# Kernel optimization log

Hardware: AMD Instinct MI355X
Metric: run time of the kernel (lower is better)

The kernel has to match this reference:

```python
import jax, jax.numpy as jnp
import numpy as np

B, S, D = 4, 2048, 768
H, K = 12, 64

def setup_inputs() -> dict:
    key = jax.random.key(0)
    k1, k2, k3, k4 = jax.random.split(key, 4)
    x = jax.random.normal(k1, (B, S, D), dtype=jnp.float32)
    Wq = jax.random.normal(k2, (H, D, K), dtype=jnp.float32) * 0.02
    Wk = jax.random.normal(k3, (H, D, K), dtype=jnp.float32) * 0.02
    Wv = jax.random.normal(k4, (H, D, K), dtype=jnp.float32) * 0.02
    return {"x": x, "Wq": Wq, "Wk": Wk, "Wv": Wv}

def reference(x, Wq, Wk, Wv):
    # per-head projections (batched over heads): [B,H,S,K]
    q = jnp.einsum('bsd,hdk->bhsk', x, Wq)
    k = jnp.einsum('bsd,hdk->bhsk', x, Wk)
    v = jnp.einsum('bsd,hdk->bhsk', x, Wv)
    scale = 1.0 / jnp.sqrt(jnp.float32(q.shape[-1]))
    scores = jnp.einsum('bhsk,bhtk->bhst', q, k) * scale  # [B,H,S,S]
    causal = jnp.tril(jnp.ones((x.shape[1], x.shape[1]), dtype=bool))
    scores = jnp.where(causal, scores, jnp.float32(-jnp.inf))
    wei = jax.nn.softmax(scores, axis=-1)
    out = jnp.einsum('bhst,bhtk->bhsk', wei, v)  # [B,H,S,K]
    # concat heads on last dim, matching torch.cat([head(x)...], dim=-1)
    b, h, s, kk = out.shape
    return out.transpose(0, 2, 1, 3).reshape(b, s, h * kk)
```

## Files before the change

kernel.cpp:

```cpp
#include <hip/hip_runtime.h>
#include <math.h>

#define BB 4
#define SS 2048
#define DD 768
#define HH 12
#define KK 64

#define NPROJ 3
#define HK    (HH * KK)
#define NCOLS (NPROJ * HK)
#define MROWS (BB * SS)
#define PER   (BB * HH * SS * KK)

typedef __attribute__((ext_vector_type(8))) short bf16x8;
typedef __attribute__((ext_vector_type(4))) short bf16x4;
typedef __attribute__((ext_vector_type(4))) float f32x4;
typedef __attribute__((ext_vector_type(16))) float f32x16;

static __device__ __forceinline__ short f2bf(float f) {
  union { float f; unsigned u; } v;
  v.f = f;
  unsigned r = (v.u + 0x7fff + ((v.u >> 16) & 1)) >> 16;
  return (short)r;
}

static __device__ __forceinline__ unsigned cvtpk(float lo, float hi) {
  unsigned r;
  asm("v_cvt_pk_bf16_f32 %0, %1, %2" : "=v"(r) : "v"(lo), "v"(hi));
  return r;
}

static __device__ __forceinline__ float fexp2(float x) {
#if __has_builtin(__builtin_amdgcn_exp2f)
  return __builtin_amdgcn_exp2f(x);
#else
  return exp2f(x);
#endif
}

__global__ __launch_bounds__(256) void conv_x(const float* __restrict__ x,
                                              short* __restrict__ xbf) {
  int i = (blockIdx.x * 256 + threadIdx.x) * 4;
  float4 v = *(const float4*)(x + i);
  bf16x4 o = {f2bf(v.x), f2bf(v.y), f2bf(v.z), f2bf(v.w)};
  *(bf16x4*)(xbf + i) = o;
}

__global__ __launch_bounds__(256) void conv_w(const float* __restrict__ Wq,
                                              const float* __restrict__ Wk,
                                              const float* __restrict__ Wv,
                                              short* __restrict__ wbf) {
  int o = blockIdx.x * 256 + threadIdx.x;
  int n = o / DD, d = o % DD;
  int proj = n / HK;
  int hk = n % HK;
  int h = hk >> 6, k = hk & 63;
  const float* W = proj == 0 ? Wq : (proj == 1 ? Wk : Wv);
  float v = W[(size_t)h * DD * KK + (size_t)d * KK + k];
  if (proj == 0) v *= 0.125f * 1.44269504088896340736f;
  wbf[o] = f2bf(v);
}

__global__ __launch_bounds__(256) void qkv_gemm(const short* __restrict__ xbf,
                                                const short* __restrict__ wbf,
                                                short* __restrict__ qkv) {
  __shared__ short smem[128 * 128];
  short* As = smem;
  short* Bs = smem + 128 * 64;
  int bm = blockIdx.x & 63, bn = blockIdx.x >> 6;
  int m0 = bm * 128, n0 = bn * 128;
  int tid = threadIdx.x, lane = tid & 63, wid = tid >> 6;
  int li = lane & 15, lg = lane >> 4;
  int wm = wid >> 1, wn = wid & 1;

  f32x4 acc[4][4];
  #pragma unroll
  for (int mi = 0; mi < 4; ++mi)
    #pragma unroll
    for (int ni = 0; ni < 4; ++ni)
      acc[mi][ni] = (f32x4){0.f, 0.f, 0.f, 0.f};

  int rowoff = lane >> 3;
  int kpsw = ((lane & 7) ^ rowoff) * 8;

  for (int kt = 0; kt < DD / 64; ++kt) {
    #pragma unroll
    for (int j = 0; j < 4; ++j) {
      int eb = wid * 2048 + j * 512;
      int row = (eb >> 6) + rowoff;
      __builtin_amdgcn_global_load_lds(
          (const __attribute__((address_space(1))) void*)(
              xbf + (size_t)(m0 + row) * DD + kt * 64 + kpsw),
          (__attribute__((address_space(3))) void*)(As + eb), 16, 0, 0);
      __builtin_amdgcn_global_load_lds(
          (const __attribute__((address_space(1))) void*)(
              wbf + (size_t)(n0 + row) * DD + kt * 64 + kpsw),
          (__attribute__((address_space(3))) void*)(Bs + eb), 16, 0, 0);
    }
    __syncthreads();

    #pragma unroll
    for (int kk = 0; kk < 2; ++kk) {
      bf16x8 af[4], bfr[4];
      #pragma unroll
      for (int mi = 0; mi < 4; ++mi)
        af[mi] = *(const bf16x8*)(As + (wm * 64 + mi * 16 + li) * 64 +
                                  (((kk * 4 + lg) ^ (li & 7)) << 3));
      #pragma unroll
      for (int ni = 0; ni < 4; ++ni)
        bfr[ni] = *(const bf16x8*)(Bs + (wn * 64 + ni * 16 + li) * 64 +
                                   (((kk * 4 + lg) ^ (li & 7)) << 3));
      #pragma unroll
      for (int mi = 0; mi < 4; ++mi)
        #pragma unroll
        for (int ni = 0; ni < 4; ++ni)
          acc[mi][ni] = __builtin_amdgcn_mfma_f32_16x16x32_bf16(
              af[mi], bfr[ni], acc[mi][ni], 0, 0, 0);
    }
    __syncthreads();
  }

  int proj = n0 / HK;
  int hk0 = n0 % HK;
  int h0 = hk0 >> 6;

  if (proj == 2) {
    #pragma unroll
    for (int ni = 0; ni < 4; ++ni) {
      int ncol = n0 + wn * 64 + ni * 16 + li;
      int hk = ncol % HK;
      int h = hk >> 6, k = hk & 63;
      #pragma unroll
      for (int mi = 0; mi < 4; ++mi) {
        int mrow0 = m0 + wm * 64 + mi * 16 + lg * 4;
        int b = mrow0 >> 11, s = mrow0 & 2047;
        bf16x4 o = {f2bf(acc[mi][ni][0]), f2bf(acc[mi][ni][1]),
                    f2bf(acc[mi][ni][2]), f2bf(acc[mi][ni][3])};
        *(bf16x4*)(qkv + 2 * (size_t)PER +
                   ((size_t)(b * HH + h) * KK + k) * SS + s) = o;
      }
    }
  } else {
    short* Cs = smem;
    #pragma unroll
    for (int ni = 0; ni < 4; ++ni) {
      int nl = wn * 64 + ni * 16 + li;
      int slot = nl >> 3, nlo = nl & 7;
      #pragma unroll
      for (int mi = 0; mi < 4; ++mi) {
        int ml0 = wm * 64 + mi * 16 + lg * 4;
        #pragma unroll
        for (int r = 0; r < 4; ++r) {
          int ml = ml0 + r;
          Cs[ml * 128 + ((slot ^ (ml & 7)) << 3) + nlo] =
              f2bf(acc[mi][ni][r]);
        }
      }
    }
    __syncthreads();
    int sl = tid & 7;
    #pragma unroll
    for (int p = 0; p < 8; ++p) {
      int line = p * 32 + (tid >> 3);
      int hh = line >> 7, mrow = line & 127;
      bf16x8 v = *(const bf16x8*)&Cs[mrow * 128 +
                                     (((hh * 8 + sl) ^ (mrow & 7)) << 3)];
      int gm = m0 + mrow;
      int b = gm >> 11, s = gm & 2047;
      *(bf16x8*)(qkv + (size_t)proj * PER +
                 ((size_t)(b * HH + h0 + hh) * SS + s) * KK + sl * 8) = v;
    }
  }
}

static __device__ __forceinline__ void attn_step_lds(
    const short* Kt, const short* Vv, const bf16x8* qf, bool diag, int h2,
    int lq, int hi, float& lsum, f32x16& acc0, f32x16& acc1) {
  int x7 = lq & 7;
  bf16x8 kf[4];
  {
    int kbase = (h2 * 32 + lq) * 64;
    #pragma unroll
    for (int c = 0; c < 4; ++c)
      kf[c] = *(const bf16x8*)&Kt[kbase + (((2 * c + hi) ^ x7)) * 8];
  }
  bf16x8 vf[2][2];
  #pragma unroll
  for (int m2 = 0; m2 < 2; ++m2) {
    int vbase = (32 * m2 + lq) * 64;
    #pragma unroll
    for (int c = 0; c < 2; ++c)
      vf[m2][c] =
          *(const bf16x8*)&Vv[vbase + (((h2 * 4 + 2 * c + hi) ^ x7)) * 8];
  }

  f32x16 sc;
  #pragma unroll
  for (int r = 0; r < 16; ++r) sc[r] = 0.f;
  #pragma unroll
  for (int c = 0; c < 4; ++c)
    sc = __builtin_amdgcn_mfma_f32_32x32x16_bf16(kf[c], qf[c], sc, 0, 0, 0);

  if (diag) {
    #pragma unroll
    for (int r = 0; r < 16; ++r) {
      int crow = (r & 3) + 8 * (r >> 2) + 4 * hi;
      if (crow > lq) sc[r] = -INFINITY;
    }
  }

  float p[16];
  #pragma unroll
  for (int r = 0; r < 16; ++r) p[r] = fexp2(sc[r]);

  float s8[8];
  #pragma unroll
  for (int r = 0; r < 8; ++r) s8[r] = p[2 * r] + p[2 * r + 1];
  lsum += ((s8[0] + s8[1]) + (s8[2] + s8[3])) +
          ((s8[4] + s8[5]) + (s8[6] + s8[7]));

  bf16x8 pf[2];
  #pragma unroll
  for (int c = 0; c < 2; ++c) {
    unsigned a0u = cvtpk(p[8 * c + 0], p[8 * c + 1]);
    unsigned b0u = cvtpk(p[8 * c + 4], p[8 * c + 5]);
    unsigned a1u = cvtpk(p[8 * c + 2], p[8 * c + 3]);
    unsigned b1u = cvtpk(p[8 * c + 6], p[8 * c + 7]);
    asm volatile("v_permlane32_swap_b32 %0, %1" : "+v"(a0u), "+v"(b0u));
    asm volatile("v_permlane32_swap_b32 %0, %1" : "+v"(a1u), "+v"(b1u));
    union { unsigned u[4]; bf16x8 v; } pu;
    pu.u[0] = a0u; pu.u[1] = a1u; pu.u[2] = b0u; pu.u[3] = b1u;
    pf[c] = pu.v;
  }

  acc0 = __builtin_amdgcn_mfma_f32_32x32x16_bf16(vf[0][0], pf[0], acc0, 0, 0, 0);
  acc0 = __builtin_amdgcn_mfma_f32_32x32x16_bf16(vf[0][1], pf[1], acc0, 0, 0, 0);
  acc1 = __builtin_amdgcn_mfma_f32_32x32x16_bf16(vf[1][0], pf[0], acc1, 0, 0, 0);
  acc1 = __builtin_amdgcn_mfma_f32_32x32x16_bf16(vf[1][1], pf[1], acc1, 0, 0, 0);
}

__global__ __launch_bounds__(256) void attn_kernel(
    const short* __restrict__ qkv, float* __restrict__ out) {
  __shared__ short tile[2][8192];

  int tid = threadIdx.x;
  int wid = tid >> 6, lane = tid & 63;
  int bid = blockIdx.x;
  int qb = 15 - bid / 48;
  int bh = bid % 48;
  int b = bh / HH, h = bh % HH;
  int Q0 = qb * 128;
  int s0w = Q0 + 32 * wid;
  int lq = lane & 31, hi = lane >> 5;

  const short* Qb = qkv + (size_t)bh * SS * KK;
  const short* Kb = qkv + (size_t)PER + (size_t)bh * SS * KK;
  const short* Vt = qkv + 2 * (size_t)PER + (size_t)bh * KK * SS;

  bf16x8 qf[4];
  #pragma unroll
  for (int c = 0; c < 4; ++c)
    qf[c] = *(const bf16x8*)(Qb + (size_t)(s0w + lq) * KK + c * 16 + hi * 8);

  f32x16 acc0, acc1;
  #pragma unroll
  for (int r = 0; r < 16; ++r) { acc0[r] = 0.f; acc1[r] = 0.f; }
  float lsum = 0.f;

  int srow = tid >> 3;
  int sl2 = (tid & 7) ^ (srow & 7);
  int ldsK = wid * 512;

  const int tmax = 2 * qb + 1;

  #define STAGE(bf_, t_)                                                       \
    {                                                                          \
      int kt0 = (t_) * 64;                                                     \
      _Pragma("unroll")                                                        \
      for (int i = 0; i < 2; ++i) {                                            \
        __builtin_amdgcn_global_load_lds(                                      \
            (const __attribute__((address_space(1))) void*)(                   \
                Kb + (size_t)(kt0 + i * 32 + srow) * KK + sl2 * 8),            \
            (__attribute__((address_space(3))) void*)(&tile[bf_][i * 2048 +    \
                                                                 ldsK]),       \
            16, 0, 0);                                                         \
        __builtin_amdgcn_global_load_lds(                                      \
            (const __attribute__((address_space(1))) void*)(                   \
                Vt + (size_t)(i * 32 + srow) * SS + kt0 + sl2 * 8),            \
            (__attribute__((address_space(3))) void*)(&tile[bf_][4096 +        \
                                                                 i * 2048 +    \
                                                                 ldsK]),       \
            16, 0, 0);                                                         \
      }                                                                        \
    }

  STAGE(0, 0);

  for (int t = 0; t <= tmax; ++t) {
    int cur = t & 1;
    if (t < tmax) {
      STAGE(cur ^ 1, t + 1);
      asm volatile("s_waitcnt vmcnt(4)" ::: "memory");
    } else {
      asm volatile("s_waitcnt vmcnt(0)" ::: "memory");
    }
    __builtin_amdgcn_s_barrier();

    const short* Kt = &tile[cur][0];
    const short* Vv = &tile[cur][4096];
    int kt0 = t * 64;
    #pragma unroll
    for (int h2 = 0; h2 < 2; ++h2) {
      int ks = kt0 + 32 * h2;
      if (ks <= s0w)
        attn_step_lds(Kt, Vv, qf, ks == s0w, h2, lq, hi, lsum, acc0, acc1);
    }
    __builtin_amdgcn_s_barrier();
  }
  #undef STAGE

  lsum += __shfl_xor(lsum, 32, 64);
  float inv = 1.0f / lsum;
  float* orow = out + ((size_t)(b * SS + s0w + lq)) * HK + h * KK;
  #pragma unroll
  for (int g = 0; g < 4; ++g) {
    int kd = 8 * g + 4 * hi;
    float4 w0 = {acc0[g * 4 + 0] * inv, acc0[g * 4 + 1] * inv,
                 acc0[g * 4 + 2] * inv, acc0[g * 4 + 3] * inv};
    float4 w1 = {acc1[g * 4 + 0] * inv, acc1[g * 4 + 1] * inv,
                 acc1[g * 4 + 2] * inv, acc1[g * 4 + 3] * inv};
    *(float4*)(orow + kd) = w0;
    *(float4*)(orow + 32 + kd) = w1;
  }
}

extern "C" void kernel_launch(void* const* d_in, const int* in_sizes, int n_in,
                              void* d_out, int out_size, void* d_ws,
                              size_t ws_size, hipStream_t stream) {
  const float* x  = (const float*)d_in[0];
  const float* Wq = (const float*)d_in[1];
  const float* Wk = (const float*)d_in[2];
  const float* Wv = (const float*)d_in[3];
  short* ws  = (short*)d_ws;
  short* qkv = ws;
  short* xbf = ws + (size_t)3 * PER;
  short* wbf = xbf + (size_t)MROWS * DD;
  float* o   = (float*)d_out;

  conv_x<<<(MROWS * DD) / 4 / 256, 256, 0, stream>>>(x, xbf);
  conv_w<<<(NCOLS * DD) / 256, 256, 0, stream>>>(Wq, Wk, Wv, wbf);
  qkv_gemm<<<(MROWS / 128) * (NCOLS / 128), 256, 0, stream>>>(xbf, wbf, qkv);
  attn_kernel<<<48 * 16, 256, 0, stream>>>(ws, o);
}
```

Baseline: 111.7 us.

## Double-buffer QKV GEMM LDS tiles and remap block order for L2 locality

The QKV projection GEMM now uses two LDS buffers, so the async global-to-LDS loads for the next K tile are issued before computing on the current one, with vmcnt waits and raw barriers instead of full syncthreads. Block indices are also remapped so that consecutive blocks interleave over tile groups, which is meant to spread work and improve cache reuse across CUs. The cost is doubled LDS (64KB), which may lower occupancy, and reliance on hand-placed waitcnt counts for correctness.

```diff
diff --git a/kernel.cpp b/kernel.cpp
--- a/kernel.cpp
+++ b/kernel.cpp
@@ -65,10 +65,10 @@
 __global__ __launch_bounds__(256) void qkv_gemm(const short* __restrict__ xbf,
                                                 const short* __restrict__ wbf,
                                                 short* __restrict__ qkv) {
-  __shared__ short smem[128 * 128];
-  short* As = smem;
-  short* Bs = smem + 128 * 64;
-  int bm = blockIdx.x & 63, bn = blockIdx.x >> 6;
+  __shared__ short smem[4 * 128 * 64];
+  int bid = blockIdx.x;
+  int tile = (bid & 7) * 144 + (bid >> 3);
+  int bm = tile & 63, bn = tile >> 6;
   int m0 = bm * 128, n0 = bn * 128;
   int tid = threadIdx.x, lane = tid & 63, wid = tid >> 6;
   int li = lane & 15, lg = lane >> 4;
@@ -84,22 +84,39 @@
   int rowoff = lane >> 3;
   int kpsw = ((lane & 7) ^ rowoff) * 8;
 
+  #define GSTAGE(bf_, kt_)                                                     \
+    {                                                                          \
+      short* As_ = smem + (bf_) * 16384;                                       \
+      short* Bs_ = As_ + 8192;                                                 \
+      _Pragma("unroll")                                                        \
+      for (int j = 0; j < 4; ++j) {                                            \
+        int eb = wid * 2048 + j * 512;                                         \
+        int row = (eb >> 6) + rowoff;                                          \
+        __builtin_amdgcn_global_load_lds(                                      \
+            (const __attribute__((address_space(1))) void*)(                   \
+                xbf + (size_t)(m0 + row) * DD + (kt_) * 64 + kpsw),            \
+            (__attribute__((address_space(3))) void*)(As_ + eb), 16, 0, 0);    \
+        __builtin_amdgcn_global_load_lds(                                      \
+            (const __attribute__((address_space(1))) void*)(                   \
+                wbf + (size_t)(n0 + row) * DD + (kt_) * 64 + kpsw),            \
+            (__attribute__((address_space(3))) void*)(Bs_ + eb), 16, 0, 0);    \
+      }                                                                        \
+    }
+
+  GSTAGE(0, 0);
+
   for (int kt = 0; kt < DD / 64; ++kt) {
-    #pragma unroll
-    for (int j = 0; j < 4; ++j) {
-      int eb = wid * 2048 + j * 512;
-      int row = (eb >> 6) + rowoff;
-      __builtin_amdgcn_global_load_lds(
-          (const __attribute__((address_space(1))) void*)(
-              xbf + (size_t)(m0 + row) * DD + kt * 64 + kpsw),
-          (__attribute__((address_space(3))) void*)(As + eb), 16, 0, 0);
-      __builtin_amdgcn_global_load_lds(
-          (const __attribute__((address_space(1))) void*)(
-              wbf + (size_t)(n0 + row) * DD + kt * 64 + kpsw),
-          (__attribute__((address_space(3))) void*)(Bs + eb), 16, 0, 0);
-    }
-    __syncthreads();
-
+    int cur = kt & 1;
+    if (kt + 1 < DD / 64) {
+      GSTAGE(cur ^ 1, kt + 1);
+      asm volatile("s_waitcnt vmcnt(8)" ::: "memory");
+    } else {
+      asm volatile("s_waitcnt vmcnt(0)" ::: "memory");
+    }
+    __builtin_amdgcn_s_barrier();
+
+    const short* As = smem + cur * 16384;
+    const short* Bs = As + 8192;
     #pragma unroll
     for (int kk = 0; kk < 2; ++kk) {
       bf16x8 af[4], bfr[4];
@@ -118,8 +135,9 @@
           acc[mi][ni] = __builtin_amdgcn_mfma_f32_16x16x32_bf16(
               af[mi], bfr[ni], acc[mi][ni], 0, 0, 0);
     }
-    __syncthreads();
-  }
+    __builtin_amdgcn_s_barrier();
+  }
+  #undef GSTAGE
 
   int proj = n0 / HK;
   int hk0 = n0 % HK;
@@ -143,6 +161,7 @@
     }
   } else {
     short* Cs = smem;
+    __syncthreads();
     #pragma unroll
     for (int ni = 0; ni < 4; ++ni) {
       int nl = wn * 64 + ni * 16 + li;
```

Result: faster. 109.3 us (-2.1%).
